# Optimization experiments

Measured on AMD Instinct MI355X. Metric: run time of the kernel, lower is better.

Reference implementation:

```python
import jax, jax.numpy as jnp
import numpy as np

N_QUBITS = 12
LAYERS = 4
ENCODERS = ['angle_rx', 'angle_ry', 'h_angle_rx', 'h_angle_ry']

_INV_SQRT2 = 1.0 / np.sqrt(2.0)
H_GATE = jnp.array([[_INV_SQRT2, _INV_SQRT2], [_INV_SQRT2, -_INV_SQRT2]], dtype=jnp.complex64)


def rx_mat(t):
    # t: scalar or (B,) -> (...,2,2)
    c = jnp.cos(t / 2).astype(jnp.complex64)
    s = jnp.sin(t / 2).astype(jnp.complex64)
    return jnp.stack([jnp.stack([c, -1j * s], -1), jnp.stack([-1j * s, c], -1)], -2)


def ry_mat(t):
    c = jnp.cos(t / 2).astype(jnp.complex64)
    s = jnp.sin(t / 2).astype(jnp.complex64)
    return jnp.stack([jnp.stack([c, -s], -1), jnp.stack([s, c], -1)], -2)


def rz_mat(t):
    e = jnp.exp(-1j * t.astype(jnp.complex64) / 2)
    z = jnp.zeros_like(e)
    return jnp.stack([jnp.stack([e, z], -1), jnp.stack([z, jnp.conj(e)], -1)], -2)


def apply_1q(state, U, q, n):
    # state: (B, 2^n); wire q is axis q in big-endian (PennyLane) ordering
    B = state.shape[0]
    L, R = 2 ** q, 2 ** (n - q - 1)
    s = state.reshape(B, L, 2, R)
    if U.ndim == 2:
        s = jnp.einsum('ab,BLbR->BLaR', U, s)
    else:  # per-sample gate (B,2,2)
        s = jnp.einsum('Bab,BLbR->BLaR', U, s)
    return s.reshape(B, 2 ** n)


def apply_cnot_adjacent(state, q, n):
    # CNOT(control=q, target=q+1)
    B = state.shape[0]
    L, R = 2 ** q, 2 ** (n - q - 2)
    s = state.reshape(B, L, 2, 2, R)
    s = jnp.stack([s[:, :, 0], s[:, :, 1, ::-1]], axis=2)
    return s.reshape(B, 2 ** n)


def run_circuit(features, theta, encoder, n, layers):
    B = features.shape[0]
    state = jnp.zeros((B, 2 ** n), dtype=jnp.complex64).at[:, 0].set(1.0)
    use_h = encoder.startswith('h_')
    rot = rx_mat if encoder.endswith('rx') else ry_mat
    # encoding: one angle per qubit, batched gate
    for q in range(n):
        if use_h:
            state = apply_1q(state, H_GATE, q, n)
        state = apply_1q(state, rot(features[:, q]), q, n)
    # variational block (hadamard=False)
    for l in range(layers):
        for q in range(n):
            state = apply_1q(state, rx_mat(theta[l, q, 0]), q, n)
            state = apply_1q(state, ry_mat(theta[l, q, 1]), q, n)
            state = apply_1q(state, rz_mat(theta[l, q, 2]), q, n)
        for q in range(0, n - 1, 2):
            state = apply_cnot_adjacent(state, q, n)
        for q in range(1, n - 1, 2):
            state = apply_cnot_adjacent(state, q, n)
    # <Z_q> for every qubit
    p = jnp.abs(state) ** 2  # (B, 2^n)
    ez = []
    for q in range(n):
        pr = p.reshape(B, 2 ** q, 2, -1)
        ez.append(pr[:, :, 0].sum((1, 2)) - pr[:, :, 1].sum((1, 2)))
    return jnp.stack(ez, axis=-1)  # (B, n)


def setup_inputs() -> dict:
    key = jax.random.key(0)
    k1, k2 = jax.random.split(key)
    features = jax.random.uniform(k1, (1024, N_QUBITS), dtype=jnp.float32)
    theta = 0.01 * jax.random.normal(k2, (LAYERS, N_QUBITS, 3), dtype=jnp.float32)
    alpha = jnp.zeros((len(ENCODERS),), dtype=jnp.float32)
    return {"features": features, "theta": theta, "alpha": alpha}


def reference(features, theta, alpha):
    arch_w = jax.nn.softmax(alpha)
    branch = jnp.stack(
        [run_circuit(features, theta, enc, N_QUBITS, LAYERS) for enc in ENCODERS], axis=0
    )  # (E, B, n_qubits)
    y = jnp.einsum('e,ebq->bq', arch_w, branch)
    return y
```

## Files before the change

kernel.cpp:

```cpp
#include <hip/hip_runtime.h>
#include <math.h>

#define NQ 12
#define DIM 4096
#define NL 4
#define THREADS 256
#define SWZC(e) ((e) ^ (((e) >> 3) & 14) ^ (((e) >> 7) & 15))
#define WAVEFENCE() { __builtin_amdgcn_wave_barrier(); __builtin_amdgcn_sched_barrier(0); }

typedef float v2f __attribute__((ext_vector_type(2)));

__device__ __forceinline__ v2f pkfma(v2f a, v2f b, v2f c) {
    v2f d; asm("v_pk_fma_f32 %0, %1, %2, %3" : "=v"(d) : "v"(a), "v"(b), "v"(c)); return d;
}
__device__ __forceinline__ v2f pkmul(v2f a, v2f b) {
    v2f d; asm("v_pk_mul_f32 %0, %1, %2" : "=v"(d) : "v"(a), "v"(b)); return d;
}
__device__ __forceinline__ v2f pkadd(v2f a, v2f b) {
    v2f d; asm("v_pk_add_f32 %0, %1, %2" : "=v"(d) : "v"(a), "v"(b)); return d;
}
__device__ __forceinline__ float2 cmulS(float2 a, float2 b) {
    return make_float2(fmaf(a.x, b.x, -a.y * b.y), fmaf(a.x, b.y, a.y * b.x));
}

struct C4 { v2f r, i, ni, nr; };

#define CMUL4(orE, orI, KR, KNI, KI, xre, xim) \
    { orE = pkfma(KNI, xim, pkmul(KR, xre)); orI = pkfma(KI, xre, pkmul(KR, xim)); }
#define CMAC4(orE, orI, KR, KNI, KI, xre, xim) \
    { orE = pkfma(KR, xre, pkfma(KNI, xim, orE)); orI = pkfma(KR, xim, pkfma(KI, xre, orI)); }

#define QUADBODY(A_, B_, C_, D_) { \
    v2f z0r,z0i,z1r,z1i,z2r,z2i,z3r,z3i; \
    CMUL4(z0r,z0i, la.r, la.ni, la.i, sre[A_], sim[A_]); CMAC4(z0r,z0i, lb.r, lb.ni, lb.i, sre[B_], sim[B_]); \
    CMUL4(z1r,z1i, lb.nr, lb.ni, lb.i, sre[A_], sim[A_]); CMAC4(z1r,z1i, la.r, la.i, la.ni, sre[B_], sim[B_]); \
    CMUL4(z2r,z2i, la.r, la.ni, la.i, sre[C_], sim[C_]); CMAC4(z2r,z2i, lb.r, lb.ni, lb.i, sre[D_], sim[D_]); \
    CMUL4(z3r,z3i, lb.nr, lb.ni, lb.i, sre[C_], sim[C_]); CMAC4(z3r,z3i, la.r, la.i, la.ni, sre[D_], sim[D_]); \
    v2f y0r,y0i,y1r,y1i,y2r,y2i,y3r,y3i; \
    CMUL4(y0r,y0i, ha.r, ha.ni, ha.i, z0r, z0i); CMAC4(y0r,y0i, hb.r, hb.ni, hb.i, z2r, z2i); \
    CMUL4(y1r,y1i, ha.r, ha.ni, ha.i, z1r, z1i); CMAC4(y1r,y1i, hb.r, hb.ni, hb.i, z3r, z3i); \
    CMUL4(y2r,y2i, hb.nr, hb.ni, hb.i, z0r, z0i); CMAC4(y2r,y2i, ha.r, ha.i, ha.ni, z2r, z2i); \
    CMUL4(y3r,y3i, hb.nr, hb.ni, hb.i, z1r, z1i); CMAC4(y3r,y3i, ha.r, ha.i, ha.ni, z3r, z3i); \
    sre[A_]=y0r; sim[A_]=y0i; sre[B_]=y1r; sim[B_]=y1i; \
    sre[C_]=y3r; sim[C_]=y3i; sre[D_]=y2r; sim[D_]=y2i; }

__device__ __forceinline__ void pass_hi(v2f* sre, v2f* sim, const v2f (*U)[4]) {
    C4 la={U[0][0],U[0][1],U[0][2],U[0][3]}, lb={U[1][0],U[1][1],U[1][2],U[1][3]},
       ha={U[2][0],U[2][1],U[2][2],U[2][3]}, hb={U[3][0],U[3][1],U[3][2],U[3][3]};
    QUADBODY(0,4,8,12) QUADBODY(1,5,9,13) QUADBODY(2,6,10,14) QUADBODY(3,7,11,15)
}
__device__ __forceinline__ void pass_lo(v2f* sre, v2f* sim, const v2f (*U)[4]) {
    C4 la={U[0][0],U[0][1],U[0][2],U[0][3]}, lb={U[1][0],U[1][1],U[1][2],U[1][3]},
       ha={U[2][0],U[2][1],U[2][2],U[2][3]}, hb={U[3][0],U[3][1],U[3][2],U[3][3]};
    QUADBODY(0,1,2,3) QUADBODY(4,5,6,7) QUADBODY(8,9,10,11) QUADBODY(12,13,14,15)
}

__global__ __launch_bounds__(THREADS, 2)
void vqc_kernel(const float* __restrict__ features,
                const float* __restrict__ theta,
                const float* __restrict__ alpha,
                float* __restrict__ out)
{
    __shared__ v2f scr[DIM];
    __shared__ v2f Upk[24][4][4];
    __shared__ v2f red[12 * 4];
    __shared__ float wez[12];

    float2* cs = (float2*)scr;
    float2 (*U48)[4] = (float2(*)[4])((char*)scr + 1152);
    float2 (*enc)[2] = (float2(*)[2])((char*)scr + 2688);
    float2 (*pairT)[4] = (float2(*)[4])((char*)scr + 3072);
    float2* loc = (float2*)((char*)scr + 3456);

    const int tid = threadIdx.x;
    const bool special = (blockIdx.x == 0);
    const int gA = special ? 0 : 2 * ((int)blockIdx.x - 1);
    const int gB = gA + 1;

    if (tid < NL * NQ * 3) {
        float s, c; sincosf(0.5f * theta[tid], &s, &c);
        cs[tid] = make_float2(c, s);
    }
    if (tid >= 160 && tid < 184) {
        int c_ = (tid - 160) / 12, q = (tid - 160) % 12;
        const float r_ = 0.70710678118654752f;
        float2 a0, a1;
        if (special) { a0 = make_float2(r_, 0.f); a1 = a0; }
        else {
            int g = c_ ? gB : gA;
            int esl = g % 3, b = g / 3;
            float f = features[b * NQ + q];
            float s, c; sincosf(0.5f * f, &s, &c);
            if (esl == 0)      { a0 = make_float2(c, 0.f); a1 = make_float2(0.f, -s); }
            else if (esl == 1) { a0 = make_float2(c, 0.f); a1 = make_float2(s, 0.f); }
            else               { a0 = make_float2((c-s)*r_, 0.f); a1 = make_float2((c+s)*r_, 0.f); }
        }
        enc[c_ * NQ + q][0] = a0; enc[c_ * NQ + q][1] = a1;
    }
    __syncthreads();

    if (tid < NL * NQ) {
        float c0 = cs[tid*3+0].x, s0 = cs[tid*3+0].y;
        float c1 = cs[tid*3+1].x, s1 = cs[tid*3+1].y;
        float c2 = cs[tid*3+2].x, s2 = cs[tid*3+2].y;
        float2 a00 = make_float2( c1*c0,  s1*s0);
        float2 a01 = make_float2(-s1*c0, -c1*s0);
        float2 a10 = make_float2( s1*c0, -c1*s0);
        float2 a11 = make_float2( c1*c0, -s1*s0);
        float2 ep = make_float2(c2, -s2), em = make_float2(c2, s2);
        U48[tid][0] = cmulS(ep, a00); U48[tid][1] = cmulS(ep, a01);
        U48[tid][2] = cmulS(em, a10); U48[tid][3] = cmulS(em, a11);
    }
    if (tid >= 64 && tid < 112) {
        int x = tid - 64;
        int c_ = x / 24, y = x % 24, p = y >> 2, v = y & 3;
        pairT[c_ * 6 + p][v] = cmulS(enc[c_*NQ + 2*p][v >> 1], enc[c_*NQ + 2*p + 1][v & 1]);
    }
    __syncthreads();

    for (int idx = tid; idx < 384; idx += THREADS) {
        int p = idx >> 4, rest = idx & 15, c = rest >> 2, comp = rest & 3;
        int l = p / 6, m = p % 6;
        int q = (c < 2) ? (2*m + 1) : (2*m);
        float2 u = U48[l*NQ + q][c & 1];
        float xv = (comp == 0) ? u.x : (comp == 1) ? u.y : (comp == 2) ? -u.y : -u.x;
        v2f vv = {xv, xv};
        Upk[p][c][comp] = vv;
    }
    if (tid >= 192 && tid < 224) {
        int x = tid - 192; int c_ = x >> 4, j = x & 15;
        loc[c_ * 16 + j] = cmulS(pairT[c_*6 + 4][j >> 2], pairT[c_*6 + 5][j & 3]);
    }
    __syncthreads();

    v2f sre[16], sim[16];
    {
        int t = tid;
        float2 preA = cmulS(cmulS(pairT[0][(t>>6)&3], pairT[1][(t>>4)&3]),
                            cmulS(pairT[2][(t>>2)&3], pairT[3][t&3]));
        float2 preB = cmulS(cmulS(pairT[6][(t>>6)&3], pairT[7][(t>>4)&3]),
                            cmulS(pairT[8][(t>>2)&3], pairT[9][t&3]));
        #pragma unroll
        for (int j = 0; j < 16; ++j) {
            float2 aA = cmulS(preA, loc[j]);
            float2 aB = cmulS(preB, loc[16 + j]);
            v2f r = {aA.x, aB.x}, ii = {aA.y, aB.y};
            sre[j] = r; sim[j] = ii;
        }
    }
    __syncthreads();

    #pragma unroll 1
    for (int l = 0; l < NL; ++l) {
        pass_hi(sre, sim, Upk[l*6 + 4]);
        pass_lo(sre, sim, Upk[l*6 + 5]);
        {
            int ba = SWZC(tid << 4);
            int ib = ((tid >> 4) << 8) | (tid & 15);
            int bb = SWZC(ib);
            #pragma unroll
            for (int j = 0; j < 16; ++j) scr[ba ^ j] = sre[j];
            WAVEFENCE();
            #pragma unroll
            for (int j = 0; j < 16; ++j) sre[j] = scr[bb ^ SWZC(j << 4)];
            WAVEFENCE();
            #pragma unroll
            for (int j = 0; j < 16; ++j) scr[ba ^ j] = sim[j];
            WAVEFENCE();
            #pragma unroll
            for (int j = 0; j < 16; ++j) sim[j] = scr[bb ^ SWZC(j << 4)];
            WAVEFENCE();
        }
        pass_hi(sre, sim, Upk[l*6 + 2]);
        pass_lo(sre, sim, Upk[l*6 + 3]);
        {
            int ib = ((tid >> 4) << 8) | (tid & 15);
            int bb = SWZC(ib);
            int bc = SWZC(tid);
            #pragma unroll
            for (int j = 0; j < 16; ++j) scr[bb ^ SWZC(j << 4)] = sre[j];
            __syncthreads();
            #pragma unroll
            for (int j = 0; j < 16; ++j) sre[j] = scr[bc ^ SWZC(j << 8)];
            __syncthreads();
            #pragma unroll
            for (int j = 0; j < 16; ++j) scr[bb ^ SWZC(j << 4)] = sim[j];
            __syncthreads();
            #pragma unroll
            for (int j = 0; j < 16; ++j) sim[j] = scr[bc ^ SWZC(j << 8)];
            __syncthreads();
        }
        pass_hi(sre, sim, Upk[l*6 + 0]);
        pass_lo(sre, sim, Upk[l*6 + 1]);
        if (l < NL - 1) {
            int bc = SWZC(tid);
            int t = tid;
            int sx = (t << 4) ^ ((t & 1) << 3) ^ (((t >> 2) & 1) << 5)
                             ^ (((t >> 4) & 1) << 7) ^ (((t >> 6) & 1) << 9);
            int bs = SWZC(sx);
            #pragma unroll
            for (int j = 0; j < 16; ++j) scr[bc ^ SWZC(j << 8)] = sre[j];
            __syncthreads();
            #pragma unroll
            for (int j = 0; j < 16; ++j) { int sj = j ^ ((j >> 1) & 2); sre[j] = scr[bs ^ sj]; }
            __syncthreads();
            #pragma unroll
            for (int j = 0; j < 16; ++j) scr[bc ^ SWZC(j << 8)] = sim[j];
            __syncthreads();
            #pragma unroll
            for (int j = 0; j < 16; ++j) { int sj = j ^ ((j >> 1) & 2); sim[j] = scr[bs ^ sj]; }
            WAVEFENCE();
        }
    }

    v2f s0 = {0.f,0.f}, s1 = {0.f,0.f}, s2 = {0.f,0.f}, s3 = {0.f,0.f}, psum = {0.f,0.f};
    {
        const v2f MONE = {-1.f, -1.f};
        #pragma unroll
        for (int j = 0; j < 16; ++j) {
            v2f p = pkfma(sim[j], sim[j], pkmul(sre[j], sre[j]));
            psum = pkadd(psum, p);
            if (j & 8)                        s0 = pkfma(p, MONE, s0); else s0 = pkadd(s0, p);
            if (j & 4)                        s1 = pkfma(p, MONE, s1); else s1 = pkadd(s1, p);
            if ((((j >> 1) ^ (j >> 2)) & 1))  s2 = pkfma(p, MONE, s2); else s2 = pkadd(s2, p);
            if (j & 1)                        s3 = pkfma(p, MONE, s3); else s3 = pkadd(s3, p);
        }
    }
    v2f vals[12];
    {
        int t = tid;
        int mt = t ^ ((t >> 1) & 0xAA);
        vals[0] = s0; vals[1] = s1; vals[2] = s2; vals[3] = s3;
        vals[4]  = ((t >> 7) & 1)  ? -s3 : s3;
        vals[5]  = ((mt >> 6) & 1) ? -psum : psum;
        vals[6]  = ((mt >> 5) & 1) ? -psum : psum;
        vals[7]  = ((mt >> 4) & 1) ? -psum : psum;
        vals[8]  = ((mt >> 3) & 1) ? -psum : psum;
        vals[9]  = ((mt >> 2) & 1) ? -psum : psum;
        vals[10] = ((mt >> 1) & 1) ? -psum : psum;
        vals[11] = (mt & 1)        ? -psum : psum;
    }
    const int lane = tid & 63, wv = tid >> 6;
    #pragma unroll
    for (int q = 0; q < 12; ++q) {
        v2f v = vals[q];
        #pragma unroll
        for (int mm = 32; mm >= 1; mm >>= 1) {
            v.x += __shfl_xor(v.x, mm, 64);
            v.y += __shfl_xor(v.y, mm, 64);
        }
        if (lane == 0) red[q * 4 + wv] = v;
    }
    __syncthreads();

    if (tid < 12) {
        v2f v = pkadd(pkadd(red[tid*4+0], red[tid*4+1]), pkadd(red[tid*4+2], red[tid*4+3]));
        float A0 = alpha[0], A1 = alpha[1], A2 = alpha[2], A3 = alpha[3];
        float mx = fmaxf(fmaxf(A0, A1), fmaxf(A2, A3));
        float E0 = expf(A0-mx), E1 = expf(A1-mx), E2 = expf(A2-mx), E3 = expf(A3-mx);
        float den = E0 + E1 + E2 + E3;
        if (special) {
            wez[tid] = (E2 / den) * v.x;
        } else {
            int eslA = gA % 3, bA = gA / 3;
            int eslB = gB % 3, bB = gB / 3;
            float wA = ((eslA == 0) ? E0 : (eslA == 1) ? E1 : E3) / den;
            float wB = ((eslB == 0) ? E0 : (eslB == 1) ? E1 : E3) / den;
            atomicAdd(out + bA * NQ + tid, wA * v.x);
            atomicAdd(out + bB * NQ + tid, wB * v.y);
        }
    }
    if (special) {
        __syncthreads();
        for (int bb2 = tid; bb2 < 1024; bb2 += THREADS) {
            #pragma unroll
            for (int q = 0; q < NQ; ++q)
                atomicAdd(out + bb2 * NQ + q, wez[q]);
        }
    }
}

extern "C" void kernel_launch(void* const* d_in, const int* in_sizes, int n_in,
                              void* d_out, int out_size, void* d_ws, size_t ws_size,
                              hipStream_t stream) {
    const float* features = (const float*)d_in[0];
    const float* theta    = (const float*)d_in[1];
    const float* alpha    = (const float*)d_in[2];
    float* out = (float*)d_out;

    hipMemsetAsync(out, 0, (size_t)out_size * sizeof(float), stream);
    vqc_kernel<<<dim3(1537), THREADS, 0, stream>>>(features, theta, alpha, out);
}
```

Baseline: 139.3 us.

## Split LDS scratch into real/imag buffers to halve transpose barriers

Replaces the single shared scratch buffer with separate real and imaginary buffers, so each state transpose writes and reads both halves in one round instead of two sequential rounds. This removes about half of the block-wide barriers per layer, and the load for the next layer is moved to the top of the loop. It also hoists the swizzled index computations out of the loop and places one barrier between the two final passes to guard the buffer reuse. LDS usage doubles (another 32KB), which could reduce occupancy below the launch-bounds target of 2 blocks per CU.

```diff
diff --git a/kernel.cpp b/kernel.cpp
--- a/kernel.cpp
+++ b/kernel.cpp
@@ -61,16 +61,17 @@
                 const float* __restrict__ alpha,
                 float* __restrict__ out)
 {
-    __shared__ v2f scr[DIM];
+    __shared__ v2f scrR[DIM];
+    __shared__ v2f scrI[DIM];
     __shared__ v2f Upk[24][4][4];
     __shared__ v2f red[12 * 4];
     __shared__ float wez[12];
 
-    float2* cs = (float2*)scr;
-    float2 (*U48)[4] = (float2(*)[4])((char*)scr + 1152);
-    float2 (*enc)[2] = (float2(*)[2])((char*)scr + 2688);
-    float2 (*pairT)[4] = (float2(*)[4])((char*)scr + 3072);
-    float2* loc = (float2*)((char*)scr + 3456);
+    float2* cs = (float2*)scrR;
+    float2 (*U48)[4] = (float2(*)[4])((char*)scrR + 1152);
+    float2 (*enc)[2] = (float2(*)[2])((char*)scrR + 2688);
+    float2 (*pairT)[4] = (float2(*)[4])((char*)scrR + 3072);
+    float2* loc = (float2*)((char*)scrR + 3456);
 
     const int tid = threadIdx.x;
     const bool special = (blockIdx.x == 0);
@@ -150,66 +151,45 @@
     }
     __syncthreads();
 
+    const int ba = SWZC(tid << 4);
+    const int bb = SWZC((((tid >> 4) << 8) | (tid & 15)));
+    const int bc = SWZC(tid);
+    const int sx = (tid << 4) ^ ((tid & 1) << 3) ^ (((tid >> 2) & 1) << 5)
+                             ^ (((tid >> 4) & 1) << 7) ^ (((tid >> 6) & 1) << 9);
+    const int bs = SWZC(sx);
+
     #pragma unroll 1
     for (int l = 0; l < NL; ++l) {
+        if (l > 0) {
+            #pragma unroll
+            for (int j = 0; j < 16; ++j) {
+                int a = bs ^ (j ^ ((j >> 1) & 2));
+                sre[j] = scrR[a]; sim[j] = scrI[a];
+            }
+        }
         pass_hi(sre, sim, Upk[l*6 + 4]);
         pass_lo(sre, sim, Upk[l*6 + 5]);
-        {
-            int ba = SWZC(tid << 4);
-            int ib = ((tid >> 4) << 8) | (tid & 15);
-            int bb = SWZC(ib);
-            #pragma unroll
-            for (int j = 0; j < 16; ++j) scr[ba ^ j] = sre[j];
-            WAVEFENCE();
-            #pragma unroll
-            for (int j = 0; j < 16; ++j) sre[j] = scr[bb ^ SWZC(j << 4)];
-            WAVEFENCE();
-            #pragma unroll
-            for (int j = 0; j < 16; ++j) scr[ba ^ j] = sim[j];
-            WAVEFENCE();
-            #pragma unroll
-            for (int j = 0; j < 16; ++j) sim[j] = scr[bb ^ SWZC(j << 4)];
-            WAVEFENCE();
-        }
+        WAVEFENCE();
+        #pragma unroll
+        for (int j = 0; j < 16; ++j) { int a = ba ^ j; scrR[a] = sre[j]; scrI[a] = sim[j]; }
+        WAVEFENCE();
+        #pragma unroll
+        for (int j = 0; j < 16; ++j) { int a = bb ^ SWZC(j << 4); sre[j] = scrR[a]; sim[j] = scrI[a]; }
         pass_hi(sre, sim, Upk[l*6 + 2]);
         pass_lo(sre, sim, Upk[l*6 + 3]);
-        {
-            int ib = ((tid >> 4) << 8) | (tid & 15);
-            int bb = SWZC(ib);
-            int bc = SWZC(tid);
-            #pragma unroll
-            for (int j = 0; j < 16; ++j) scr[bb ^ SWZC(j << 4)] = sre[j];
-            __syncthreads();
-            #pragma unroll
-            for (int j = 0; j < 16; ++j) sre[j] = scr[bc ^ SWZC(j << 8)];
-            __syncthreads();
-            #pragma unroll
-            for (int j = 0; j < 16; ++j) scr[bb ^ SWZC(j << 4)] = sim[j];
-            __syncthreads();
-            #pragma unroll
-            for (int j = 0; j < 16; ++j) sim[j] = scr[bc ^ SWZC(j << 8)];
-            __syncthreads();
-        }
+        WAVEFENCE();
+        #pragma unroll
+        for (int j = 0; j < 16; ++j) { int a = bb ^ SWZC(j << 4); scrR[a] = sre[j]; scrI[a] = sim[j]; }
+        __syncthreads();
+        #pragma unroll
+        for (int j = 0; j < 16; ++j) { int a = bc ^ SWZC(j << 8); sre[j] = scrR[a]; sim[j] = scrI[a]; }
         pass_hi(sre, sim, Upk[l*6 + 0]);
+        if (l < NL - 1) __syncthreads();
         pass_lo(sre, sim, Upk[l*6 + 1]);
         if (l < NL - 1) {
-            int bc = SWZC(tid);
-            int t = tid;
-            int sx = (t << 4) ^ ((t & 1) << 3) ^ (((t >> 2) & 1) << 5)
-                             ^ (((t >> 4) & 1) << 7) ^ (((t >> 6) & 1) << 9);
-            int bs = SWZC(sx);
             #pragma unroll
-            for (int j = 0; j < 16; ++j) scr[bc ^ SWZC(j << 8)] = sre[j];
+            for (int j = 0; j < 16; ++j) { int a = bc ^ SWZC(j << 8); scrR[a] = sre[j]; scrI[a] = sim[j]; }
             __syncthreads();
-            #pragma unroll
-            for (int j = 0; j < 16; ++j) { int sj = j ^ ((j >> 1) & 2); sre[j] = scr[bs ^ sj]; }
-            __syncthreads();
-            #pragma unroll
-            for (int j = 0; j < 16; ++j) scr[bc ^ SWZC(j << 8)] = sim[j];
-            __syncthreads();
-            #pragma unroll
-            for (int j = 0; j < 16; ++j) { int sj = j ^ ((j >> 1) & 2); sim[j] = scr[bs ^ sj]; }
-            WAVEFENCE();
         }
     }
 
```

New measurement: 139.4 us. No clear change (+0.1%).
